# Optimization experiments

Hardware: AMD Instinct MI355X
Metric: run time of the kernel (lower is better)

The kernel has to match this reference:

```python
import jax, jax.numpy as jnp
import numpy as np

CE_W, TRI_W, CEN_W, ALN_W, BAL_W = 1.0, 1.0, 0.0005, 0.5, 0.1
LS_EPS = 0.1      # label smoothing
MARGIN = 0.3      # triplet margin
F_ALPHA, F_GAMMA = 0.25, 2.0


def setup_inputs() -> dict:
    key = jax.random.key(0)
    ks = jax.random.split(key, 7)
    B, C, D = 1024, 8000, 2048
    return {
        "logits": jax.random.normal(ks[0], (B, C), jnp.float32),
        "features": jax.random.normal(ks[1], (B, D), jnp.float32),
        "feat_rgb": jax.random.normal(ks[2], (B, D), jnp.float32),
        "feat_ir": jax.random.normal(ks[3], (B, D), jnp.float32),
        "modality_weights": jax.random.uniform(ks[4], (B, 2), jnp.float32),
        "centers": jax.random.uniform(ks[5], (C, D), jnp.float32, -1.0, 1.0),
        "labels": jax.random.randint(ks[6], (B,), 0, 64),
    }


def reference(logits, features, feat_rgb, feat_ir, modality_weights, centers, labels):
    B, C = logits.shape
    logp = jax.nn.log_softmax(logits, axis=-1)                      # [B, C]
    logp_y = jnp.take_along_axis(logp, labels[:, None], axis=1)[:, 0]
    # CrossEntropy with label smoothing 0.1 (torch semantics)
    ce = jnp.mean(-(1.0 - LS_EPS) * logp_y - LS_EPS * jnp.mean(logp, axis=-1))
    # Focal loss (faithful to source: uses logpt, so term is <= 0)
    ce_ns = -logp_y
    pt = jnp.exp(-ce_ns)
    focal = jnp.mean(F_ALPHA * (1.0 - pt) ** F_GAMMA * (-ce_ns))
    # Batch-hard triplet (vectorized replacement for per-row python loop)
    sq = jnp.sum(features ** 2, axis=1)
    d2 = jnp.maximum(sq[:, None] + sq[None, :] - 2.0 * (features @ features.T), 0.0)
    dist = jnp.where(d2 > 0, jnp.sqrt(jnp.where(d2 > 0, d2, 1.0)), 0.0)  # safe sqrt
    eq = labels[:, None] == labels[None, :]
    eye = jnp.eye(B, dtype=bool)
    pos_mask = eq & ~eye
    neg_mask = ~eq
    hp = jnp.max(jnp.where(pos_mask, dist, -1.0), axis=1)   # hardest positive
    hn = jnp.min(jnp.where(neg_mask, dist, 1e9), axis=1)    # hardest negative
    valid = jnp.any(pos_mask, axis=1) & jnp.any(neg_mask, axis=1)
    tl = jax.nn.relu(hp - hn + MARGIN)
    triplet = jnp.sum(jnp.where(valid, tl, 0.0)) / jnp.maximum(jnp.sum(valid), 1)
    # Center loss (centers gathered and detached)
    cen = jnp.mean((features - jax.lax.stop_gradient(centers[labels])) ** 2)
    # Modality alignment (single rgb-ir pair): mean(1 - cos)
    f1 = feat_rgb / jnp.maximum(jnp.linalg.norm(feat_rgb, axis=1, keepdims=True), 1e-12)
    f2 = feat_ir / jnp.maximum(jnp.linalg.norm(feat_ir, axis=1, keepdims=True), 1e-12)
    align = jnp.mean(1.0 - jnp.sum(f1 * f2, axis=1))
    # Modality balance: max_entropy - entropy
    ent = jnp.mean(-jnp.sum(modality_weights * jnp.log(modality_weights + 1e-8), axis=1))
    balance = jnp.log(jnp.float32(modality_weights.shape[1])) - ent
    # Modality consistency: mse to detached mean over modalities
    mean_feat = jax.lax.stop_gradient(0.5 * (feat_rgb + feat_ir))
    cons = 0.5 * (jnp.mean((feat_rgb - mean_feat) ** 2) + jnp.mean((feat_ir - mean_feat) ** 2))
    total = (CE_W * (0.7 * ce + 0.3 * focal) + TRI_W * triplet + CEN_W * cen
             + ALN_W * align + BAL_W * balance + 0.1 * cons)
    return jnp.stack([total, ce, focal, triplet, cen, align, balance, cons])
```

## Files before the change

### kernel.cpp

```cpp
#include <hip/hip_runtime.h>
#include <math.h>

#define NB 1024
#define NC 8000
#define ND 2048

#define WS_SQ   0
#define WS_CE   1024
#define WS_FO   2048
#define WS_CEN  3072
#define WS_AL   4096
#define WS_CO   5120
#define WS_HPM  6144
#define WS_HNM  22528
#define WS_FB_BYTES 262144

#define NDIST 512
#define NT    32

typedef __attribute__((ext_vector_type(8))) short bf16x8;
typedef __attribute__((ext_vector_type(4))) float f32x4;
#define GLOB __attribute__((address_space(1)))
#define LDSP __attribute__((address_space(3)))

__device__ inline unsigned short f2bf(float f) {
    unsigned u = __float_as_uint(f);
    u += 0x7FFFu + ((u >> 16) & 1u);
    return (unsigned short)(u >> 16);
}

__global__ __launch_bounds__(256) void k_feat(const float* __restrict__ F,
                                              const float* __restrict__ RGB,
                                              const float* __restrict__ IR,
                                              const float* __restrict__ CEN,
                                              const int* __restrict__ labels,
                                              float* __restrict__ ws,
                                              unsigned short* __restrict__ Fb) {
    const int tid = threadIdx.x;
    const int lane = tid & 63, wid = tid >> 6;
    const int row = blockIdx.x * 4 + wid;
    const float4* f4 = (const float4*)(F + (size_t)row * ND);
    const float4* c4 = (const float4*)(CEN + (size_t)labels[row] * ND);
    const float4* r4 = (const float4*)(RGB + (size_t)row * ND);
    const float4* g4 = (const float4*)(IR + (size_t)row * ND);
    ushort4* fb4 = (ushort4*)(Fb + (size_t)row * ND);

    float s_ff = 0, s_fc = 0, s_rr = 0, s_ii = 0, s_ri = 0, s_dd = 0;
#pragma unroll 4
    for (int t = 0; t < (ND / 4) / 64; ++t) {
        const int q = t * 64 + lane;
        float4 f = f4[q], c = c4[q], r = r4[q], g = g4[q];
        ushort4 h;
        h.x = f2bf(f.x); h.y = f2bf(f.y); h.z = f2bf(f.z); h.w = f2bf(f.w);
        fb4[q] = h;
        float fa[4] = {f.x, f.y, f.z, f.w};
        float ca[4] = {c.x, c.y, c.z, c.w};
        float ra[4] = {r.x, r.y, r.z, r.w};
        float ga[4] = {g.x, g.y, g.z, g.w};
#pragma unroll
        for (int k = 0; k < 4; ++k) {
            s_ff = fmaf(fa[k], fa[k], s_ff);
            float d = fa[k] - ca[k];
            s_fc = fmaf(d, d, s_fc);
            s_rr = fmaf(ra[k], ra[k], s_rr);
            s_ii = fmaf(ga[k], ga[k], s_ii);
            s_ri = fmaf(ra[k], ga[k], s_ri);
            float e = ra[k] - ga[k];
            s_dd = fmaf(e, e, s_dd);
        }
    }
#pragma unroll
    for (int off = 32; off > 0; off >>= 1) {
        s_ff += __shfl_down(s_ff, off);
        s_fc += __shfl_down(s_fc, off);
        s_rr += __shfl_down(s_rr, off);
        s_ii += __shfl_down(s_ii, off);
        s_ri += __shfl_down(s_ri, off);
        s_dd += __shfl_down(s_dd, off);
    }
    if (lane == 0) {
        ws[WS_SQ + row] = s_ff;
        ws[WS_CEN + row] = s_fc;
        float nr = fmaxf(sqrtf(s_rr), 1e-12f);
        float ni = fmaxf(sqrtf(s_ii), 1e-12f);
        ws[WS_AL + row] = 1.0f - s_ri / (nr * ni);
        ws[WS_CO + row] = s_dd;
    }
}

__global__ __launch_bounds__(256) void k_main(const unsigned short* __restrict__ Fb,
                                              const float* __restrict__ logits,
                                              const int* __restrict__ labels,
                                              float* __restrict__ ws) {
    __shared__ __align__(16) unsigned short As[3][32 * 64];
    __shared__ __align__(16) unsigned short Bs[3][64 * 64];
    __shared__ int lr[32], lc[64];
    __shared__ float sqr[32], sqc[64], hpl[32], hnl[32];
    __shared__ float rs[4], rsx[4];

    const int tid = threadIdx.x;
    const int lane = tid & 63, wid = tid >> 6;

    if (blockIdx.x < NDIST) {
        const int d = blockIdx.x;
        const int xcd = d & 7, loc = d >> 3;
        const int rp = (xcd >> 1) * 8 + (loc & 7);
        const int cb = (xcd & 1) * 8 + (loc >> 3);
        const int row0 = rp << 5, col0 = cb << 6;
        const float* sq = ws + WS_SQ;

        if (tid < 32) {
            lr[tid] = labels[row0 + tid];
            sqr[tid] = sq[row0 + tid];
            hpl[tid] = -1.0f;
            hnl[tid] = 1e9f;
        } else if (tid >= 64 && tid < 128) {
            int t = tid - 64;
            lc[t] = labels[col0 + t];
            sqc[t] = sq[col0 + t];
        }

        const int r8 = lane >> 3;
        const int sl = lane & 7;
        const int soEl = ((sl ^ r8) * 8);

#define STAGE(IT, BUF) do {                                                              \
    const int k0_ = (IT) * 64;                                                           \
    __builtin_amdgcn_global_load_lds(                                                    \
        (const GLOB unsigned int*)(Fb + (size_t)(row0 + wid * 8 + r8) * ND + k0_ + soEl),\
        (LDSP unsigned int*)&As[BUF][(wid * 8) * 64], 16, 0, 0);                         \
    _Pragma("unroll")                                                                    \
    for (int t = 0; t < 2; ++t) {                                                        \
        const int rb_ = wid * 16 + t * 8;                                                \
        __builtin_amdgcn_global_load_lds(                                                \
            (const GLOB unsigned int*)(Fb + (size_t)(col0 + rb_ + r8) * ND + k0_ + soEl),\
            (LDSP unsigned int*)&Bs[BUF][rb_ * 64], 16, 0, 0);                           \
    }                                                                                    \
} while (0)

        const int wr = wid >> 1, wc = wid & 1;
        f32x4 acc[2] = {};

        STAGE(0, 0);
        STAGE(1, 1);
        STAGE(2, 2);
        int cur = 0;
#pragma unroll 1
        for (int it = 0; it < NT; ++it) {
            if (it <= NT - 3)      asm volatile("s_waitcnt vmcnt(6)" ::: "memory");
            else if (it == NT - 2) asm volatile("s_waitcnt vmcnt(3)" ::: "memory");
            else                   asm volatile("s_waitcnt vmcnt(0)" ::: "memory");
            __builtin_amdgcn_sched_barrier(0);
            __builtin_amdgcn_s_barrier();

            const char* Ab = (const char*)&As[cur][0];
            const char* Bb = (const char*)&Bs[cur][0];
#pragma unroll
            for (int kk = 0; kk < 2; ++kk) {
                const int kb = kk * 64 + (lane >> 4) * 16;
                const int xo = (lane & 7) << 4;
                const int rt = wr * 16 + (lane & 15);
                bf16x8 a = *(const bf16x8*)(Ab + rt * 128 + (kb ^ xo));
                bf16x8 b[2];
#pragma unroll
                for (int ni = 0; ni < 2; ++ni) {
                    const int ct = wc * 32 + ni * 16 + (lane & 15);
                    b[ni] = *(const bf16x8*)(Bb + ct * 128 + (kb ^ xo));
                }
#pragma unroll
                for (int ni = 0; ni < 2; ++ni)
                    acc[ni] = __builtin_amdgcn_mfma_f32_16x16x32_bf16(a, b[ni], acc[ni], 0, 0, 0);
            }

            __builtin_amdgcn_sched_barrier(0);
            __builtin_amdgcn_s_barrier();
            if (it + 3 < NT) STAGE(it + 3, cur);
            cur = (cur == 2) ? 0 : cur + 1;
        }
#undef STAGE

#pragma unroll
        for (int reg = 0; reg < 4; ++reg) {
            const int rt = wr * 16 + (lane >> 4) * 4 + reg;
            const int lbr = lr[rt];
            const float sr = sqr[rt];
            float myhp = -1.0f, myhn = 1e9f;
#pragma unroll
            for (int ni = 0; ni < 2; ++ni) {
                const int ct = wc * 32 + ni * 16 + (lane & 15);
                float d2 = sr + sqc[ct] - 2.0f * acc[ni][reg];
                float dist = sqrtf(fmaxf(d2, 0.0f));
                if (row0 + rt != col0 + ct) {
                    if (lbr == lc[ct]) myhp = fmaxf(myhp, dist);
                    else               myhn = fminf(myhn, dist);
                }
            }
#pragma unroll
            for (int off = 1; off < 16; off <<= 1) {
                myhp = fmaxf(myhp, __shfl_xor(myhp, off, 16));
                myhn = fminf(myhn, __shfl_xor(myhn, off, 16));
            }
            if ((lane & 15) == 0) {
                atomicMax((int*)&hpl[rt], __float_as_int(myhp));
                atomicMin((int*)&hnl[rt], __float_as_int(myhn));
            }
        }
        __syncthreads();
        if (tid < 32) {
            ws[WS_HPM + (size_t)(row0 + tid) * 16 + cb] = hpl[tid];
            ws[WS_HNM + (size_t)(row0 + tid) * 16 + cb] = hnl[tid];
        }
    } else {
        const int row = blockIdx.x - NDIST;
        const float* x = logits + (size_t)row * NC;
        const float4* x4 = (const float4*)x;
        float xl = 0.0f;
        if (tid == 0) xl = x[labels[row]];

        float s = 0.0f, sx = 0.0f;
        for (int q = tid; q < NC / 4; q += 256) {
            float4 v = x4[q];
            float vv[4] = {v.x, v.y, v.z, v.w};
#pragma unroll
            for (int c = 0; c < 4; ++c) {
                sx += vv[c];
                s += __expf(vv[c]);
            }
        }
#pragma unroll
        for (int off = 32; off > 0; off >>= 1) {
            s  += __shfl_down(s, off);
            sx += __shfl_down(sx, off);
        }
        if (lane == 0) { rs[wid] = s; rsx[wid] = sx; }
        __syncthreads();
        if (tid == 0) {
            s = rs[0] + rs[1] + rs[2] + rs[3];
            sx = rsx[0] + rsx[1] + rsx[2] + rsx[3];
            const float lse = __logf(s);
            const float logp_y = xl - lse;
            const float mean_logp = sx * (1.0f / NC) - lse;
            const float pt = __expf(logp_y);
            ws[WS_CE + row] = -(1.0f - 0.1f) * logp_y - 0.1f * mean_logp;
            ws[WS_FO + row] = 0.25f * (1.0f - pt) * (1.0f - pt) * logp_y;
        }
    }
}

__global__ __launch_bounds__(256) void k_fin(const float* __restrict__ mw,
                                             float* __restrict__ ws,
                                             float* __restrict__ out) {
    const int tid = threadIdx.x;
    float sum_tl = 0.0f, ent = 0.0f, sce = 0.0f, sfo = 0.0f;
    float scen = 0.0f, sal = 0.0f, sco = 0.0f;
    int cnt = 0;
#pragma unroll
    for (int t = 0; t < 4; ++t) {
        const int i = tid + t * 256;
        const float4* hp4 = (const float4*)(ws + WS_HPM + (size_t)i * 16);
        const float4* hn4 = (const float4*)(ws + WS_HNM + (size_t)i * 16);
        float h1 = -1.0f, h2 = 1e9f;
#pragma unroll
        for (int c = 0; c < 4; ++c) {
            float4 p = hp4[c], n = hn4[c];
            h1 = fmaxf(h1, fmaxf(fmaxf(p.x, p.y), fmaxf(p.z, p.w)));
            h2 = fminf(h2, fminf(fminf(n.x, n.y), fminf(n.z, n.w)));
        }
        if (h1 >= 0.0f && h2 < 1e8f) { sum_tl += fmaxf(h1 - h2 + 0.3f, 0.0f); cnt++; }
        sce += ws[WS_CE + i];
        sfo += ws[WS_FO + i];
        scen += ws[WS_CEN + i];
        sal += ws[WS_AL + i];
        sco += ws[WS_CO + i];
        float w0 = mw[2 * i], w1 = mw[2 * i + 1];
        ent -= w0 * __logf(w0 + 1e-8f) + w1 * __logf(w1 + 1e-8f);
    }
#pragma unroll
    for (int off = 32; off > 0; off >>= 1) {
        sum_tl += __shfl_down(sum_tl, off);
        ent += __shfl_down(ent, off);
        sce += __shfl_down(sce, off);
        sfo += __shfl_down(sfo, off);
        scen += __shfl_down(scen, off);
        sal += __shfl_down(sal, off);
        sco += __shfl_down(sco, off);
        cnt += __shfl_down(cnt, off);
    }
    __shared__ float red[4][7];
    __shared__ int rc[4];
    const int lane = tid & 63, wid = tid >> 6;
    if (lane == 0) {
        red[wid][0] = sum_tl; red[wid][1] = ent; red[wid][2] = sce; red[wid][3] = sfo;
        red[wid][4] = scen; red[wid][5] = sal; red[wid][6] = sco;
        rc[wid] = cnt;
    }
    __syncthreads();
    if (tid == 0) {
#pragma unroll
        for (int w = 1; w < 4; ++w) {
            red[0][0] += red[w][0]; red[0][1] += red[w][1]; red[0][2] += red[w][2];
            red[0][3] += red[w][3]; red[0][4] += red[w][4]; red[0][5] += red[w][5];
            red[0][6] += red[w][6];
            rc[0] += rc[w];
        }
        const float ce = red[0][2] * (1.0f / NB);
        const float focal = red[0][3] * (1.0f / NB);
        const float triplet = red[0][0] / (float)(rc[0] > 0 ? rc[0] : 1);
        const float cen = red[0][4] * (1.0f / ((float)NB * ND));
        const float align = red[0][5] * (1.0f / NB);
        const float balance = logf(2.0f) - red[0][1] * (1.0f / NB);
        const float cons = 0.25f * red[0][6] * (1.0f / ((float)NB * ND));
        const float total = 1.0f * (0.7f * ce + 0.3f * focal) + 1.0f * triplet
                          + 0.0005f * cen + 0.5f * align + 0.1f * balance + 0.1f * cons;
        out[0] = total; out[1] = ce; out[2] = focal; out[3] = triplet;
        out[4] = cen; out[5] = align; out[6] = balance; out[7] = cons;
    }
}

extern "C" void kernel_launch(void* const* d_in, const int* in_sizes, int n_in,
                              void* d_out, int out_size, void* d_ws, size_t ws_size,
                              hipStream_t stream) {
    const float* logits   = (const float*)d_in[0];
    const float* features = (const float*)d_in[1];
    const float* feat_rgb = (const float*)d_in[2];
    const float* feat_ir  = (const float*)d_in[3];
    const float* mw       = (const float*)d_in[4];
    const float* centers  = (const float*)d_in[5];
    const int*   labels   = (const int*)d_in[6];
    float* ws  = (float*)d_ws;
    unsigned short* Fb = (unsigned short*)((char*)d_ws + WS_FB_BYTES);
    float* out = (float*)d_out;

    k_feat<<<dim3(NB / 4), dim3(256), 0, stream>>>(features, feat_rgb, feat_ir,
                                                   centers, labels, ws, Fb);
    k_main<<<dim3(NDIST + NB), dim3(256), 0, stream>>>(Fb, logits, labels, ws);
    k_fin<<<dim3(1), dim3(256), 0, stream>>>(mw, ws, out);
}
```

Baseline: 38.18 us.

## Fold final reduction into main kernel and rebalance CE rows across kernels

The single-block finalize kernel is removed. Its reduction now runs in whichever block of the main kernel arrives last, detected with a global atomic counter that the first kernel resets. The first 256 cross-entropy rows move into the feature-preprocessing kernel, so the two heavy kernels carry more even loads. This cuts one kernel launch and its tail, at the cost of a threadfence and an atomic in every main-kernel block.

Measured after the change: 134.1 us. 251% more time.

```diff
diff --git a/kernel.cpp b/kernel.cpp
--- a/kernel.cpp
+++ b/kernel.cpp
@@ -13,10 +13,13 @@
 #define WS_CO   5120
 #define WS_HPM  6144
 #define WS_HNM  22528
+#define WS_CNT  38912
 #define WS_FB_BYTES 262144
 
 #define NDIST 512
 #define NT    32
+#define NCE1  256
+#define GRID2 (NDIST + (NB - NCE1))
 
 typedef __attribute__((ext_vector_type(8))) short bf16x8;
 typedef __attribute__((ext_vector_type(4))) float f32x4;
@@ -29,74 +32,128 @@
     return (unsigned short)(u >> 16);
 }
 
-__global__ __launch_bounds__(256) void k_feat(const float* __restrict__ F,
-                                              const float* __restrict__ RGB,
-                                              const float* __restrict__ IR,
-                                              const float* __restrict__ CEN,
-                                              const int* __restrict__ labels,
-                                              float* __restrict__ ws,
-                                              unsigned short* __restrict__ Fb) {
+__device__ __forceinline__ void ce_row(int row, const float* __restrict__ logits,
+                                       const int* __restrict__ labels,
+                                       float* __restrict__ ws,
+                                       float* rs, float* rsx) {
     const int tid = threadIdx.x;
     const int lane = tid & 63, wid = tid >> 6;
-    const int row = blockIdx.x * 4 + wid;
-    const float4* f4 = (const float4*)(F + (size_t)row * ND);
-    const float4* c4 = (const float4*)(CEN + (size_t)labels[row] * ND);
-    const float4* r4 = (const float4*)(RGB + (size_t)row * ND);
-    const float4* g4 = (const float4*)(IR + (size_t)row * ND);
-    ushort4* fb4 = (ushort4*)(Fb + (size_t)row * ND);
-
-    float s_ff = 0, s_fc = 0, s_rr = 0, s_ii = 0, s_ri = 0, s_dd = 0;
+    const float* x = logits + (size_t)row * NC;
+    const float4* x4 = (const float4*)x;
+    float xl = 0.0f;
+    if (tid == 0) xl = x[labels[row]];
+
+    float s = 0.0f, sx = 0.0f;
+    for (int q = tid; q < NC / 4; q += 256) {
+        float4 v = x4[q];
+        float vv[4] = {v.x, v.y, v.z, v.w};
+#pragma unroll
+        for (int c = 0; c < 4; ++c) {
+            sx += vv[c];
+            s += __expf(vv[c]);
+        }
+    }
+#pragma unroll
+    for (int off = 32; off > 0; off >>= 1) {
+        s  += __shfl_down(s, off);
+        sx += __shfl_down(sx, off);
+    }
+    if (lane == 0) { rs[wid] = s; rsx[wid] = sx; }
+    __syncthreads();
+    if (tid == 0) {
+        s = rs[0] + rs[1] + rs[2] + rs[3];
+        sx = rsx[0] + rsx[1] + rsx[2] + rsx[3];
+        const float lse = __logf(s);
+        const float logp_y = xl - lse;
+        const float mean_logp = sx * (1.0f / NC) - lse;
+        const float pt = __expf(logp_y);
+        ws[WS_CE + row] = -(1.0f - 0.1f) * logp_y - 0.1f * mean_logp;
+        ws[WS_FO + row] = 0.25f * (1.0f - pt) * (1.0f - pt) * logp_y;
+    }
+}
+
+__global__ __launch_bounds__(256) void k_pre(const float* __restrict__ logits,
+                                             const float* __restrict__ F,
+                                             const float* __restrict__ RGB,
+                                             const float* __restrict__ IR,
+                                             const float* __restrict__ CEN,
+                                             const int* __restrict__ labels,
+                                             float* __restrict__ ws,
+                                             unsigned short* __restrict__ Fb) {
+    __shared__ float rs[4], rsx[4];
+    const int tid = threadIdx.x;
+    const int lane = tid & 63, wid = tid >> 6;
+
+    if (blockIdx.x == 0 && tid == 0) ((int*)ws)[WS_CNT] = 0;
+
+    if (blockIdx.x < 256) {
+        const int row = blockIdx.x * 4 + wid;
+        const float4* f4 = (const float4*)(F + (size_t)row * ND);
+        const float4* c4 = (const float4*)(CEN + (size_t)labels[row] * ND);
+        const float4* r4 = (const float4*)(RGB + (size_t)row * ND);
+        const float4* g4 = (const float4*)(IR + (size_t)row * ND);
+        ushort4* fb4 = (ushort4*)(Fb + (size_t)row * ND);
+
+        float s_ff = 0, s_fc = 0, s_rr = 0, s_ii = 0, s_ri = 0, s_dd = 0;
 #pragma unroll 4
-    for (int t = 0; t < (ND / 4) / 64; ++t) {
-        const int q = t * 64 + lane;
-        float4 f = f4[q], c = c4[q], r = r4[q], g = g4[q];
-        ushort4 h;
-        h.x = f2bf(f.x); h.y = f2bf(f.y); h.z = f2bf(f.z); h.w = f2bf(f.w);
-        fb4[q] = h;
-        float fa[4] = {f.x, f.y, f.z, f.w};
-        float ca[4] = {c.x, c.y, c.z, c.w};
-        float ra[4] = {r.x, r.y, r.z, r.w};
-        float ga[4] = {g.x, g.y, g.z, g.w};
-#pragma unroll
-        for (int k = 0; k < 4; ++k) {
-            s_ff = fmaf(fa[k], fa[k], s_ff);
-            float d = fa[k] - ca[k];
-            s_fc = fmaf(d, d, s_fc);
-            s_rr = fmaf(ra[k], ra[k], s_rr);
-            s_ii = fmaf(ga[k], ga[k], s_ii);
-            s_ri = fmaf(ra[k], ga[k], s_ri);
-            float e = ra[k] - ga[k];
-            s_dd = fmaf(e, e, s_dd);
-        }
-    }
-#pragma unroll
-    for (int off = 32; off > 0; off >>= 1) {
-        s_ff += __shfl_down(s_ff, off);
-        s_fc += __shfl_down(s_fc, off);
-        s_rr += __shfl_down(s_rr, off);
-        s_ii += __shfl_down(s_ii, off);
-        s_ri += __shfl_down(s_ri, off);
-        s_dd += __shfl_down(s_dd, off);
-    }
-    if (lane == 0) {
-        ws[WS_SQ + row] = s_ff;
-        ws[WS_CEN + row] = s_fc;
-        float nr = fmaxf(sqrtf(s_rr), 1e-12f);
-        float ni = fmaxf(sqrtf(s_ii), 1e-12f);
-        ws[WS_AL + row] = 1.0f - s_ri / (nr * ni);
-        ws[WS_CO + row] = s_dd;
+        for (int t = 0; t < (ND / 4) / 64; ++t) {
+            const int q = t * 64 + lane;
+            float4 f = f4[q], c = c4[q], r = r4[q], g = g4[q];
+            ushort4 h;
+            h.x = f2bf(f.x); h.y = f2bf(f.y); h.z = f2bf(f.z); h.w = f2bf(f.w);
+            fb4[q] = h;
+            float fa[4] = {f.x, f.y, f.z, f.w};
+            float ca[4] = {c.x, c.y, c.z, c.w};
+            float ra[4] = {r.x, r.y, r.z, r.w};
+            float ga[4] = {g.x, g.y, g.z, g.w};
+#pragma unroll
+            for (int k = 0; k < 4; ++k) {
+                s_ff = fmaf(fa[k], fa[k], s_ff);
+                float d = fa[k] - ca[k];
+                s_fc = fmaf(d, d, s_fc);
+                s_rr = fmaf(ra[k], ra[k], s_rr);
+                s_ii = fmaf(ga[k], ga[k], s_ii);
+                s_ri = fmaf(ra[k], ga[k], s_ri);
+                float e = ra[k] - ga[k];
+                s_dd = fmaf(e, e, s_dd);
+            }
+        }
+#pragma unroll
+        for (int off = 32; off > 0; off >>= 1) {
+            s_ff += __shfl_down(s_ff, off);
+            s_fc += __shfl_down(s_fc, off);
+            s_rr += __shfl_down(s_rr, off);
+            s_ii += __shfl_down(s_ii, off);
+            s_ri += __shfl_down(s_ri, off);
+            s_dd += __shfl_down(s_dd, off);
+        }
+        if (lane == 0) {
+            ws[WS_SQ + row] = s_ff;
+            ws[WS_CEN + row] = s_fc;
+            float nr = fmaxf(sqrtf(s_rr), 1e-12f);
+            float ni = fmaxf(sqrtf(s_ii), 1e-12f);
+            ws[WS_AL + row] = 1.0f - s_ri / (nr * ni);
+            ws[WS_CO + row] = s_dd;
+        }
+    } else {
+        ce_row(blockIdx.x - 256, logits, labels, ws, rs, rsx);
     }
 }
 
 __global__ __launch_bounds__(256) void k_main(const unsigned short* __restrict__ Fb,
                                               const float* __restrict__ logits,
                                               const int* __restrict__ labels,
-                                              float* __restrict__ ws) {
+                                              const float* __restrict__ mw,
+                                              float* __restrict__ ws,
+                                              float* __restrict__ out) {
     __shared__ __align__(16) unsigned short As[3][32 * 64];
     __shared__ __align__(16) unsigned short Bs[3][64 * 64];
     __shared__ int lr[32], lc[64];
     __shared__ float sqr[32], sqc[64], hpl[32], hnl[32];
     __shared__ float rs[4], rsx[4];
+    __shared__ float red[4][7];
+    __shared__ int rc[4];
+    __shared__ int isLast;
 
     const int tid = threadIdx.x;
     const int lane = tid & 63, wid = tid >> 6;
@@ -211,46 +268,19 @@
             ws[WS_HNM + (size_t)(row0 + tid) * 16 + cb] = hnl[tid];
         }
     } else {
-        const int row = blockIdx.x - NDIST;
-        const float* x = logits + (size_t)row * NC;
-        const float4* x4 = (const float4*)x;
-        float xl = 0.0f;
-        if (tid == 0) xl = x[labels[row]];
-
-        float s = 0.0f, sx = 0.0f;
-        for (int q = tid; q < NC / 4; q += 256) {
-            float4 v = x4[q];
-            float vv[4] = {v.x, v.y, v.z, v.w};
-#pragma unroll
-            for (int c = 0; c < 4; ++c) {
-                sx += vv[c];
-                s += __expf(vv[c]);
-            }
-        }
-#pragma unroll
-        for (int off = 32; off > 0; off >>= 1) {
-            s  += __shfl_down(s, off);
-            sx += __shfl_down(sx, off);
-        }
-        if (lane == 0) { rs[wid] = s; rsx[wid] = sx; }
-        __syncthreads();
-        if (tid == 0) {
-            s = rs[0] + rs[1] + rs[2] + rs[3];
-            sx = rsx[0] + rsx[1] + rsx[2] + rsx[3];
-            const float lse = __logf(s);
-            const float logp_y = xl - lse;
-            const float mean_logp = sx * (1.0f / NC) - lse;
-            const float pt = __expf(logp_y);
-            ws[WS_CE + row] = -(1.0f - 0.1f) * logp_y - 0.1f * mean_logp;
-            ws[WS_FO + row] = 0.25f * (1.0f - pt) * (1.0f - pt) * logp_y;
-        }
-    }
-}
-
-__global__ __launch_bounds__(256) void k_fin(const float* __restrict__ mw,
-                                             float* __restrict__ ws,
-                                             float* __restrict__ out) {
-    const int tid = threadIdx.x;
+        ce_row(NCE1 + (blockIdx.x - NDIST), logits, labels, ws, rs, rsx);
+    }
+
+    __threadfence();
+    __syncthreads();
+    if (tid == 0) {
+        int old = atomicAdd((int*)ws + WS_CNT, 1);
+        isLast = (old == GRID2 - 1);
+    }
+    __syncthreads();
+    if (!isLast) return;
+    __threadfence();
+
     float sum_tl = 0.0f, ent = 0.0f, sce = 0.0f, sfo = 0.0f;
     float scen = 0.0f, sal = 0.0f, sco = 0.0f;
     int cnt = 0;
@@ -286,9 +316,6 @@
         sco += __shfl_down(sco, off);
         cnt += __shfl_down(cnt, off);
     }
-    __shared__ float red[4][7];
-    __shared__ int rc[4];
-    const int lane = tid & 63, wid = tid >> 6;
     if (lane == 0) {
         red[wid][0] = sum_tl; red[wid][1] = ent; red[wid][2] = sce; red[wid][3] = sfo;
         red[wid][4] = scen; red[wid][5] = sal; red[wid][6] = sco;
@@ -331,8 +358,7 @@
     unsigned short* Fb = (unsigned short*)((char*)d_ws + WS_FB_BYTES);
     float* out = (float*)d_out;
 
-    k_feat<<<dim3(NB / 4), dim3(256), 0, stream>>>(features, feat_rgb, feat_ir,
-                                                   centers, labels, ws, Fb);
-    k_main<<<dim3(NDIST + NB), dim3(256), 0, stream>>>(Fb, logits, labels, ws);
-    k_fin<<<dim3(1), dim3(256), 0, stream>>>(mw, ws, out);
-}
+    k_pre<<<dim3(512), dim3(256), 0, stream>>>(logits, features, feat_rgb, feat_ir,
+                                               centers, labels, ws, Fb);
+    k_main<<<dim3(GRID2), dim3(256), 0, stream>>>(Fb, logits, labels, mw, ws, out);
+}
```
